# Kernel tuning notes

Measured on AMD Instinct MI355X. Metric: run time of the kernel, lower is better.

## Reference

```python
import jax, jax.numpy as jnp
import numpy as np

HIDDEN = 1024
HEADS = 16
HEAD_DIM = HIDDEN // HEADS  # 64
ROPE_DIM = 64
ROPE_BASE = 10000.0
B, T = 2, 2048


def setup_inputs() -> dict:
    key = jax.random.key(0)
    k1, k2, k3, k4, k5, k6 = jax.random.split(key, 6)
    x = jax.random.normal(k1, (B, T, HIDDEN), dtype=jnp.float32)
    input_ids = jax.random.randint(k2, (B, T), 0, 32000)
    # torch Linear weights: [out_features, in_features]
    qkv_w = jax.random.normal(k3, (3 * HIDDEN, HIDDEN), dtype=jnp.float32) * (1.0 / np.sqrt(HIDDEN))
    qkv_b = jnp.zeros((3 * HIDDEN,), dtype=jnp.float32)
    out_w = jax.random.normal(k4, (HIDDEN, HIDDEN), dtype=jnp.float32) * (1.0 / np.sqrt(HIDDEN))
    out_b = jnp.zeros((HIDDEN,), dtype=jnp.float32)
    global_idx = jnp.array([0, 1, 2], dtype=jnp.int64)  # special_tokens values
    return {"x": x, "input_ids": input_ids, "qkv_w": qkv_w, "qkv_b": qkv_b,
            "out_w": out_w, "out_b": out_b, "global_idx": global_idx}


def _rope_cos_sin(t, offset=0):
    inv_freq = 1.0 / (ROPE_BASE ** (jnp.arange(0, ROPE_DIM, 2, dtype=jnp.float32) / ROPE_DIM))  # [ROPE_DIM/2]
    pos = jnp.arange(offset, offset + t, dtype=jnp.float32)
    freqs = pos[:, None] * inv_freq[None, :]  # [T, ROPE_DIM/2]
    return jnp.cos(freqs)[None, None], jnp.sin(freqs)[None, None]  # [1,1,T,ROPE_DIM/2]


def _apply_rotary(x, cos, sin):
    x_rot, x_pass = x[..., :ROPE_DIM], x[..., ROPE_DIM:]
    half = ROPE_DIM // 2
    x1, x2 = x_rot[..., :half], x_rot[..., half:]
    return jnp.concatenate([x1 * cos - x2 * sin, x1 * sin + x2 * cos, x_pass], axis=-1)


def reference(x, input_ids, qkv_w, qkv_b, out_w, out_b, global_idx):
    b, t, _ = x.shape
    qkv = x @ qkv_w.T + qkv_b  # [B,T,3*HIDDEN]
    q, k, v = jnp.split(qkv, 3, axis=-1)
    # -> [B, H, T, Dh]
    reshape = lambda z: z.reshape(b, t, HEADS, HEAD_DIM).transpose(0, 2, 1, 3)
    q, k, v = reshape(q), reshape(k), reshape(v)
    cos, sin = _rope_cos_sin(t)
    q = _apply_rotary(q, cos, sin)
    k = _apply_rotary(k, cos, sin)
    # causal + global-query mask
    causal = jnp.tril(jnp.ones((t, t), dtype=bool))[None, None]  # [1,1,T,T]
    global_mask = jnp.isin(input_ids, global_idx)  # [B,T]
    allow = causal | global_mask[:, None, :, None]  # [B,1,T,T]
    scale = jnp.sqrt(jnp.float32(HEAD_DIM))
    logits = jnp.einsum('bhqd,bhkd->bhqk', q, k) / scale
    neg = -jnp.finfo(logits.dtype).max
    logits = jnp.where(allow, logits, neg)
    attn = jax.nn.softmax(logits, axis=-1)
    out = jnp.einsum('bhqk,bhkd->bhqd', attn, v)  # [B,H,T,Dh]
    out = out.transpose(0, 2, 1, 3).reshape(b, t, HEADS * HEAD_DIM)
    return out @ out_w.T + out_b
```

## Files before the change

kernel.cpp:

```cpp
#include <hip/hip_runtime.h>
#include <hip/hip_bf16.h>
#include <math.h>

typedef __bf16 bf16;
typedef __bf16 bf16x4 __attribute__((ext_vector_type(4)));
typedef __bf16 bf16x8 __attribute__((ext_vector_type(8)));
typedef float floatx4 __attribute__((ext_vector_type(4)));

#define HIDDEN 1024
#define NHEADS 16
#define HDIM 64
#define TSEQ 2048
#define NBATCH 2
#define MTOT (NBATCH * TSEQ)

__device__ inline void glds16(bf16* lds, const bf16* g)
{
  __builtin_amdgcn_global_load_lds(
      (const __attribute__((address_space(1))) unsigned int*)g,
      (__attribute__((address_space(3))) unsigned int*)lds, 16, 0, 0);
}

__global__ __launch_bounds__(256) void prep_kernel(
    const float* __restrict__ x, bf16* __restrict__ xb,
    const float* __restrict__ qkv_w, bf16* __restrict__ qkv_wb,
    float2* __restrict__ rope)
{
  const int bid = blockIdx.x;
  if (bid >= 3584) {
    const int e0 = ((bid - 3584) * 256 + threadIdx.x) * 4;
    const int t = e0 >> 5;
    const int d2 = e0 & 31;
#pragma unroll
    for (int j = 0; j < 4; j++) {
      const float inv = exp2f((float)(d2 + j) * -0.41524100f);
      float s, c;
      sincosf((float)t * inv, &s, &c);
      rope[e0 + j] = make_float2(c, s);
    }
    return;
  }
  const float* src = (bid < 2048) ? x : qkv_w;
  bf16* dst = (bid < 2048) ? xb : qkv_wb;
  const int i = (((bid < 2048) ? bid : bid - 2048) * 256 + threadIdx.x) * 8;
  const floatx4 u = *(const floatx4*)(src + i);
  const floatx4 v = *(const floatx4*)(src + i + 4);
  bf16x8 r;
#pragma unroll
  for (int j = 0; j < 4; j++) { r[j] = (bf16)u[j]; r[4 + j] = (bf16)v[j]; }
  *(bf16x8*)(dst + i) = r;
}

__global__ __launch_bounds__(256) void cvt_f32_bf16(
    const float* __restrict__ src, bf16* __restrict__ dst, int n)
{
  const int i = (blockIdx.x * 256 + threadIdx.x) * 8;
  if (i >= n) return;
  const floatx4 u = *(const floatx4*)(src + i);
  const floatx4 v = *(const floatx4*)(src + i + 4);
  bf16x8 r;
#pragma unroll
  for (int j = 0; j < 4; j++) { r[j] = (bf16)u[j]; r[4 + j] = (bf16)v[j]; }
  *(bf16x8*)(dst + i) = r;
}


#define GEMM_PROLOGUE()                                                     \
  const int tid  = threadIdx.x;                                             \
  const int lane = tid & 63;                                                \
  const int wv   = tid >> 6;                                                \
  const int quad = lane >> 4;                                               \
  const int l16  = lane & 15;                                               \
  const int m0 = blockIdx.y * 128;                                          \
  const int n0 = blockIdx.x * 128;                                          \
  const int wm = (wv >> 1) * 64;                                            \
  const int wn = (wv & 1) * 64;                                             \
  const int srow = lane >> 2;                                               \
  const int scol = ((lane & 3) ^ ((lane >> 3) & 3)) * 8;   \
  const int qsw  = (quad ^ ((l16 >> 1) & 3)) * 8;         \
  const bf16* ga0 = A + (size_t)(m0 + wv * 32 + srow) * K + scol;           \
  const bf16* gb0 = W + (size_t)(n0 + wv * 32 + srow) * K + scol;           \
  floatx4 acc[4][4];                                                        \
  _Pragma("unroll") for (int i = 0; i < 4; i++)                             \
      _Pragma("unroll") for (int j = 0; j < 4; j++)                         \
          acc[i][j] = (floatx4){0.f, 0.f, 0.f, 0.f};

#define STAGE(buf, kk)                                                      \
  glds16(&As[buf][(wv * 32) * 32], ga0 + (kk));                             \
  glds16(&As[buf][(wv * 32 + 16) * 32], ga0 + (size_t)16 * K + (kk));       \
  glds16(&Bs[buf][(wv * 32) * 32], gb0 + (kk));                             \
  glds16(&Bs[buf][(wv * 32 + 16) * 32], gb0 + (size_t)16 * K + (kk));

#define COMPUTE(buf)                                                        \
  {                                                                         \
    bf16x8 af[4], bfr[4];                                                   \
    _Pragma("unroll") for (int i = 0; i < 4; i++)                           \
        af[i] = *(const bf16x8*)(&As[buf][(wm + i * 16 + l16) * 32 + qsw]); \
    _Pragma("unroll") for (int j = 0; j < 4; j++)                           \
        bfr[j] = *(const bf16x8*)(&Bs[buf][(wn + j * 16 + l16) * 32 + qsw]);\
    _Pragma("unroll") for (int i = 0; i < 4; i++)                           \
        _Pragma("unroll") for (int j = 0; j < 4; j++)                       \
            acc[i][j] = __builtin_amdgcn_mfma_f32_16x16x32_bf16(            \
                af[i], bfr[j], acc[i][j], 0, 0, 0);                         \
  }

#define GEMM_MAIN_LOOP()                                                    \
  STAGE(0, 0);                                                              \
  STAGE(1, 32);                                                             \
  int cur = 0;                                                              \
  const int nsteps = K / 32;                                                \
  _Pragma("unroll 1") for (int t = 0; t < nsteps - 1; t++) {                \
    asm volatile("s_waitcnt vmcnt(4)" ::: "memory");                        \
    __builtin_amdgcn_s_barrier();                                           \
    if (t + 2 < nsteps) {                                                   \
      const int nb = (cur >= 1) ? cur - 1 : cur + 2;                        \
      STAGE(nb, (t + 2) * 32);                                              \
    }                                                                       \
    COMPUTE(cur);                                                           \
    cur = (cur == 2) ? 0 : cur + 1;                                         \
  }                                                                         \
  asm volatile("s_waitcnt vmcnt(0)" ::: "memory");                          \
  __builtin_amdgcn_s_barrier();                                             \
  COMPUTE(cur);

__global__ __launch_bounds__(256) void gemm_qkv(
    const bf16* __restrict__ A, const bf16* __restrict__ W,
    const float* __restrict__ bias, const float2* __restrict__ rope,
    bf16* __restrict__ Qb, bf16* __restrict__ Kb, bf16* __restrict__ Vt,
    int M, int N, int K)
{
  __shared__ bf16 As[3][128 * 32];
  __shared__ bf16 Bs[3][128 * 32];

  GEMM_PROLOGUE();
  GEMM_MAIN_LOOP();

  const int sect = n0 >> 10;
  const int hw   = ((n0 & 1023) + wn) >> 6;

  float bs[4];
#pragma unroll
  for (int j = 0; j < 4; j++) bs[j] = bias[n0 + wn + j * 16 + l16];

  if (sect < 2) {
    bf16* dst = sect ? Kb : Qb;
#pragma unroll
    for (int i = 0; i < 4; i++) {
      const int gmBase = m0 + wm + i * 16 + quad * 4;
#pragma unroll
      for (int r = 0; r < 4; r++) {
        const int gm = gmBase + r;
        const int b_ = gm >> 11, t = gm & 2047;
        const size_t rowbase = ((size_t)(b_ * NHEADS + hw) * TSEQ + t) * HDIM;
        const float2 cs0 = rope[t * 32 + l16];
        const float2 cs1 = rope[t * 32 + 16 + l16];
        const float x1a = acc[i][0][r] + bs[0];
        const float x2a = acc[i][2][r] + bs[2];
        const float x1b = acc[i][1][r] + bs[1];
        const float x2b = acc[i][3][r] + bs[3];
        dst[rowbase + l16]      = (bf16)(x1a * cs0.x - x2a * cs0.y);
        dst[rowbase + 32 + l16] = (bf16)(x1a * cs0.y + x2a * cs0.x);
        dst[rowbase + 16 + l16] = (bf16)(x1b * cs1.x - x2b * cs1.y);
        dst[rowbase + 48 + l16] = (bf16)(x1b * cs1.y + x2b * cs1.x);
      }
    }
  } else {
#pragma unroll
    for (int j = 0; j < 4; j++) {
      const int d = j * 16 + l16;
#pragma unroll
      for (int i = 0; i < 4; i++) {
        const int gmBase = m0 + wm + i * 16 + quad * 4;
        const int b_ = gmBase >> 11, t0 = gmBase & 2047;
        bf16x4 vv;
#pragma unroll
        for (int r = 0; r < 4; r++) vv[r] = (bf16)(acc[i][j][r] + bs[j]);
        *(bf16x4*)(Vt + ((size_t)((b_ * NHEADS + hw) * HDIM + d)) * TSEQ + t0) = vv;
      }
    }
  }
}

__global__ __launch_bounds__(256) void gemm_out(
    const bf16* __restrict__ A, const bf16* __restrict__ W,
    const float* __restrict__ bias, float* __restrict__ C,
    int M, int N, int K)
{
  __shared__ bf16 As[3][128 * 32];
  __shared__ bf16 Bs[3][128 * 32];

  GEMM_PROLOGUE();
  GEMM_MAIN_LOOP();

#pragma unroll
  for (int i = 0; i < 4; i++) {
    const int gmBase = m0 + wm + i * 16 + quad * 4;
#pragma unroll
    for (int j = 0; j < 4; j++) {
      const int gn = n0 + wn + j * 16 + l16;
      const float bsv = bias[gn];
#pragma unroll
      for (int r = 0; r < 4; r++)
        C[(size_t)(gmBase + r) * N + gn] = acc[i][j][r] + bsv;
    }
  }
}

__device__ inline int swz(int g) { return (g & ~7) | ((g ^ (g >> 3) ^ (g >> 6)) & 7); }

__global__ __launch_bounds__(256) void attn_kernel(
    const bf16* __restrict__ Q, const bf16* __restrict__ K,
    const bf16* __restrict__ Vt, bf16* __restrict__ O,
    const int* __restrict__ ids, const int* __restrict__ gidx)
{
  __shared__ bf16 Ks[4096];
  __shared__ bf16 Vs[4096];
  __shared__ int flags[4];

  const int tid  = threadIdx.x;
  const int lane = tid & 63;
  const int wv   = tid >> 6;
  const int quad = lane >> 4;
  const int l16  = lane & 15;

  const int xcd = blockIdx.x & 7;
  const int j   = blockIdx.x >> 3;
  const int bh  = xcd * 4 + (j >> 4);
  const int p   = j & 15;
  const int b  = bh >> 4;
  const int h  = bh & 15;

  const bf16* Qp = Q + (size_t)bh * TSEQ * HDIM;
  const bf16* Kp = K + (size_t)bh * TSEQ * HDIM;
  const bf16* Vp = Vt + (size_t)bh * HDIM * TSEQ;

  const int rK  = tid >> 3;
  const int dcK = tid & 7;
  const int gk = ((rK >> 2) & 1) * 128 + (dcK >> 2) * 64 +
                 ((dcK & 3) * 16 + (((rK >> 3) << 2) | (rK & 3)));
  const int kd0 = swz(gk) * 8, kd1 = swz(gk + 256) * 8;
  const int dV = tid >> 3;
  const int uV = tid & 7;
  const int gv = (uV >> 2) * 256 + (dV >> 4) * 64 + ((uV & 3) * 16 + (dV & 15));
  const int vd0 = swz(gv) * 8, vd1 = swz(gv + 128) * 8;

  const int g0v = gidx[0], g1v = gidx[1], g2v = gidx[2];

#pragma unroll
  for (int ph = 0; ph < 2; ph++) {
    const int qt = ph ? p : (31 - p);
    const int q0 = qt * 64 + wv * 16;

    const bf16x8 qf0 = *(const bf16x8*)(Qp + (size_t)(q0 + l16) * HDIM + quad * 8);
    const bf16x8 qf1 = *(const bf16x8*)(Qp + (size_t)(q0 + l16) * HDIM + 32 + quad * 8);

    const int myq = q0 + l16;
    const int myid = ids[b * TSEQ + myq];
    const int gl = (myid == g0v) | (myid == g1v) | (myid == g2v);
    flags[wv] = __any(gl);
    __syncthreads();
    const int anyg = flags[0] | flags[1] | flags[2] | flags[3];
    const int kmax = anyg ? TSEQ : (qt * 64 + 64);

    float lsum = 0.f;
    floatx4 o[4];
#pragma unroll
    for (int nt = 0; nt < 4; nt++) o[nt] = (floatx4){0.f, 0.f, 0.f, 0.f};

    bf16x8 kA = *(const bf16x8*)(Kp + tid * 8);
    bf16x8 kB = *(const bf16x8*)(Kp + 2048 + tid * 8);
    bf16x8 vA = *(const bf16x8*)(Vp + (size_t)dV * TSEQ + uV * 8);
    bf16x8 vB = *(const bf16x8*)(Vp + (size_t)(dV + 32) * TSEQ + uV * 8);

    for (int k0 = 0; k0 < kmax; k0 += 64) {
      __syncthreads();
      *(bf16x8*)(Ks + kd0) = kA;
      *(bf16x8*)(Ks + kd1) = kB;
      *(bf16x8*)(Vs + vd0) = vA;
      *(bf16x8*)(Vs + vd1) = vB;
      __syncthreads();

      if (k0 + 64 < kmax) {
        const bf16* kc = Kp + (size_t)(k0 + 64) * HDIM;
        kA = *(const bf16x8*)(kc + tid * 8);
        kB = *(const bf16x8*)(kc + 2048 + tid * 8);
        vA = *(const bf16x8*)(Vp + (size_t)dV * TSEQ + k0 + 64 + uV * 8);
        vB = *(const bf16x8*)(Vp + (size_t)(dV + 32) * TSEQ + k0 + 64 + uV * 8);
      }

#pragma unroll
      for (int g = 0; g < 2; g++) {
        const int kb = k0 + g * 32;
        const int rb = g * 256 + lane;
        const bf16x8 a00 = *(const bf16x8*)(Ks + swz(rb) * 8);
        const bf16x8 a01 = *(const bf16x8*)(Ks + swz(rb + 64) * 8);
        const bf16x8 a10 = *(const bf16x8*)(Ks + swz(rb + 128) * 8);
        const bf16x8 a11 = *(const bf16x8*)(Ks + swz(rb + 192) * 8);
        floatx4 s0 = (floatx4){0.f, 0.f, 0.f, 0.f};
        floatx4 s1 = (floatx4){0.f, 0.f, 0.f, 0.f};
        s0 = __builtin_amdgcn_mfma_f32_16x16x32_bf16(a00, qf0, s0, 0, 0, 0);
        s0 = __builtin_amdgcn_mfma_f32_16x16x32_bf16(a01, qf1, s0, 0, 0, 0);
        s1 = __builtin_amdgcn_mfma_f32_16x16x32_bf16(a10, qf0, s1, 0, 0, 0);
        s1 = __builtin_amdgcn_mfma_f32_16x16x32_bf16(a11, qf1, s1, 0, 0, 0);

        bf16x8 pf;
#pragma unroll
        for (int r = 0; r < 4; r++) {
          const int key0 = kb + quad * 8 + r;
          const int key1 = key0 + 4;
          const float p0 = (gl || key0 <= myq) ? __expf(s0[r] * 0.125f) : 0.f;
          const float p1 = (gl || key1 <= myq) ? __expf(s1[r] * 0.125f) : 0.f;
          lsum += p0 + p1;
          pf[r]     = (bf16)p0;
          pf[4 + r] = (bf16)p1;
        }

#pragma unroll
        for (int nt = 0; nt < 4; nt++) {
          const bf16x8 vf = *(const bf16x8*)(Vs + swz(g * 256 + nt * 64 + lane) * 8);
          o[nt] = __builtin_amdgcn_mfma_f32_16x16x32_bf16(pf, vf, o[nt], 0, 0, 0);
        }
      }
    }

    lsum += __shfl_xor(lsum, 16);
    lsum += __shfl_xor(lsum, 32);

#pragma unroll
    for (int r = 0; r < 4; r++) {
      const float inv = 1.0f / __shfl(lsum, quad * 4 + r);
      const int q = q0 + quad * 4 + r;
      const size_t rowoff = ((size_t)b * TSEQ + q) * HIDDEN + h * HDIM;
#pragma unroll
      for (int nt = 0; nt < 4; nt++)
        O[rowoff + nt * 16 + l16] = (bf16)(o[nt][r] * inv);
    }
  }
}

extern "C" void kernel_launch(void* const* d_in, const int* in_sizes, int n_in,
                              void* d_out, int out_size, void* d_ws, size_t ws_size,
                              hipStream_t stream)
{
  const float* x     = (const float*)d_in[0];
  const int*   ids   = (const int*)d_in[1];
  const float* qkv_w = (const float*)d_in[2];
  const float* qkv_b = (const float*)d_in[3];
  const float* out_w = (const float*)d_in[4];
  const float* out_b = (const float*)d_in[5];
  const int*   gidx  = (const int*)d_in[6];
  float* out = (float*)d_out;

  char* ws = (char*)d_ws;
  bf16* Q      = (bf16*)(ws);
  bf16* Kb     = (bf16*)(ws + (size_t)(8u << 20));
  bf16* Vt     = (bf16*)(ws + (size_t)(16u << 20));
  bf16* slot24 = (bf16*)(ws + (size_t)(24u << 20));
  bf16* xb     = slot24;
  bf16* O      = slot24;
  bf16* out_wb = (bf16*)(ws + (size_t)(16u << 20));
  bf16* qkv_wb = (bf16*)d_out;
  float2* rope = (float2*)((char*)d_out + (size_t)(6u << 20));

  prep_kernel<<<3648, 256, 0, stream>>>(x, xb, qkv_w, qkv_wb, rope);
  gemm_qkv<<<dim3(3072 / 128, MTOT / 128), 256, 0, stream>>>(
      xb, qkv_wb, qkv_b, rope, Q, Kb, Vt, MTOT, 3 * HIDDEN, HIDDEN);
  attn_kernel<<<512, 256, 0, stream>>>(Q, Kb, Vt, O, ids, gidx);
  cvt_f32_bf16<<<512, 256, 0, stream>>>(out_w, out_wb, HIDDEN * HIDDEN);
  gemm_out<<<dim3(HIDDEN / 128, MTOT / 128), 256, 0, stream>>>(
      O, out_wb, out_b, out, MTOT, HIDDEN, HIDDEN);
}
```

Baseline: 203.0 us.

## Remap GEMM blocks per XCD and halve out-projection N tile

Both GEMMs switch to a 1D grid whose block index is remapped so that blocks landing on the same XCD (assigned round-robin by blockIdx mod 8) cover a compact 2D region of the output. This is meant to improve L2 reuse of the A and W tiles within each XCD. The output-projection GEMM also moves from 128x128 to 128x64 tiles, doubling its grid to 512 blocks so the GPU's CUs are better occupied. The cost is more A-tile reloads and fewer MFMAs per LDS load in gemm_out, and the mapping is hardcoded to these exact grid shapes.

Result: faster. 198.7 us (-2.1%).

```diff
diff --git a/kernel.cpp b/kernel.cpp
--- a/kernel.cpp
+++ b/kernel.cpp
@@ -64,26 +64,6 @@
   *(bf16x8*)(dst + i) = r;
 }
 
-
-#define GEMM_PROLOGUE()                                                     \
-  const int tid  = threadIdx.x;                                             \
-  const int lane = tid & 63;                                                \
-  const int wv   = tid >> 6;                                                \
-  const int quad = lane >> 4;                                               \
-  const int l16  = lane & 15;                                               \
-  const int m0 = blockIdx.y * 128;                                          \
-  const int n0 = blockIdx.x * 128;                                          \
-  const int wm = (wv >> 1) * 64;                                            \
-  const int wn = (wv & 1) * 64;                                             \
-  const int srow = lane >> 2;                                               \
-  const int scol = ((lane & 3) ^ ((lane >> 3) & 3)) * 8;   \
-  const int qsw  = (quad ^ ((l16 >> 1) & 3)) * 8;         \
-  const bf16* ga0 = A + (size_t)(m0 + wv * 32 + srow) * K + scol;           \
-  const bf16* gb0 = W + (size_t)(n0 + wv * 32 + srow) * K + scol;           \
-  floatx4 acc[4][4];                                                        \
-  _Pragma("unroll") for (int i = 0; i < 4; i++)                             \
-      _Pragma("unroll") for (int j = 0; j < 4; j++)                         \
-          acc[i][j] = (floatx4){0.f, 0.f, 0.f, 0.f};
 
 #define STAGE(buf, kk)                                                      \
   glds16(&As[buf][(wv * 32) * 32], ga0 + (kk));                             \
@@ -104,25 +84,6 @@
                 af[i], bfr[j], acc[i][j], 0, 0, 0);                         \
   }
 
-#define GEMM_MAIN_LOOP()                                                    \
-  STAGE(0, 0);                                                              \
-  STAGE(1, 32);                                                             \
-  int cur = 0;                                                              \
-  const int nsteps = K / 32;                                                \
-  _Pragma("unroll 1") for (int t = 0; t < nsteps - 1; t++) {                \
-    asm volatile("s_waitcnt vmcnt(4)" ::: "memory");                        \
-    __builtin_amdgcn_s_barrier();                                           \
-    if (t + 2 < nsteps) {                                                   \
-      const int nb = (cur >= 1) ? cur - 1 : cur + 2;                        \
-      STAGE(nb, (t + 2) * 32);                                              \
-    }                                                                       \
-    COMPUTE(cur);                                                           \
-    cur = (cur == 2) ? 0 : cur + 1;                                         \
-  }                                                                         \
-  asm volatile("s_waitcnt vmcnt(0)" ::: "memory");                          \
-  __builtin_amdgcn_s_barrier();                                             \
-  COMPUTE(cur);
-
 __global__ __launch_bounds__(256) void gemm_qkv(
     const bf16* __restrict__ A, const bf16* __restrict__ W,
     const float* __restrict__ bias, const float2* __restrict__ rope,
@@ -132,8 +93,53 @@
   __shared__ bf16 As[3][128 * 32];
   __shared__ bf16 Bs[3][128 * 32];
 
-  GEMM_PROLOGUE();
-  GEMM_MAIN_LOOP();
+  const int tid  = threadIdx.x;
+  const int lane = tid & 63;
+  const int wv   = tid >> 6;
+  const int quad = lane >> 4;
+  const int l16  = lane & 15;
+
+  const int f   = blockIdx.x;
+  const int xcd = f & 7;
+  const int rr  = f >> 3;
+  const int bx  = (xcd & 1) * 12 + (rr % 12);
+  const int by  = (xcd >> 1) * 8 + (rr / 12);
+  const int m0 = by * 128;
+  const int n0 = bx * 128;
+
+  const int wm = (wv >> 1) * 64;
+  const int wn = (wv & 1) * 64;
+  const int srow = lane >> 2;
+  const int scol = ((lane & 3) ^ ((lane >> 3) & 3)) * 8;
+  const int qsw  = (quad ^ ((l16 >> 1) & 3)) * 8;
+
+  const bf16* ga0 = A + (size_t)(m0 + wv * 32 + srow) * K + scol;
+  const bf16* gb0 = W + (size_t)(n0 + wv * 32 + srow) * K + scol;
+
+  floatx4 acc[4][4];
+#pragma unroll
+  for (int i = 0; i < 4; i++)
+#pragma unroll
+    for (int j = 0; j < 4; j++) acc[i][j] = (floatx4){0.f, 0.f, 0.f, 0.f};
+
+  STAGE(0, 0);
+  STAGE(1, 32);
+  int cur = 0;
+  const int nsteps = K / 32;
+#pragma unroll 1
+  for (int t = 0; t < nsteps - 1; t++) {
+    asm volatile("s_waitcnt vmcnt(4)" ::: "memory");
+    __builtin_amdgcn_s_barrier();
+    if (t + 2 < nsteps) {
+      const int nb = (cur >= 1) ? cur - 1 : cur + 2;
+      STAGE(nb, (t + 2) * 32);
+    }
+    COMPUTE(cur);
+    cur = (cur == 2) ? 0 : cur + 1;
+  }
+  asm volatile("s_waitcnt vmcnt(0)" ::: "memory");
+  __builtin_amdgcn_s_barrier();
+  COMPUTE(cur);
 
   const int sect = n0 >> 10;
   const int hw   = ((n0 & 1023) + wn) >> 6;
@@ -187,17 +193,79 @@
     int M, int N, int K)
 {
   __shared__ bf16 As[3][128 * 32];
-  __shared__ bf16 Bs[3][128 * 32];
-
-  GEMM_PROLOGUE();
-  GEMM_MAIN_LOOP();
-
-#pragma unroll
-  for (int i = 0; i < 4; i++) {
+  __shared__ bf16 Bs[3][64 * 32];
+
+  const int tid  = threadIdx.x;
+  const int lane = tid & 63;
+  const int wv   = tid >> 6;
+  const int quad = lane >> 4;
+  const int l16  = lane & 15;
+
+  const int f   = blockIdx.x;
+  const int xcd = f & 7;
+  const int rr  = f >> 3;
+  const int bx  = (xcd & 1) * 8 + (rr & 7);
+  const int by  = (xcd >> 1) * 8 + (rr >> 3);
+  const int m0 = by * 128;
+  const int n0 = bx * 64;
+  const int wm = wv * 32;
+
+  const int srow = lane >> 2;
+  const int scol = ((lane & 3) ^ ((lane >> 3) & 3)) * 8;
+  const int qsw  = (quad ^ ((l16 >> 1) & 3)) * 8;
+
+  const bf16* ga0 = A + (size_t)(m0 + wv * 32 + srow) * K + scol;
+  const bf16* gb0 = W + (size_t)(n0 + wv * 16 + srow) * K + scol;
+
+  floatx4 acc[2][4];
+#pragma unroll
+  for (int i = 0; i < 2; i++)
+#pragma unroll
+    for (int j = 0; j < 4; j++) acc[i][j] = (floatx4){0.f, 0.f, 0.f, 0.f};
+
+#define STAGE_O(buf, kk)                                                    \
+  glds16(&As[buf][(wv * 32) * 32], ga0 + (kk));                             \
+  glds16(&As[buf][(wv * 32 + 16) * 32], ga0 + (size_t)16 * K + (kk));       \
+  glds16(&Bs[buf][(wv * 16) * 32], gb0 + (kk));
+
+#define COMPUTE_O(buf)                                                      \
+  {                                                                         \
+    bf16x8 af[2], bfr[4];                                                   \
+    _Pragma("unroll") for (int i = 0; i < 2; i++)                           \
+        af[i] = *(const bf16x8*)(&As[buf][(wm + i * 16 + l16) * 32 + qsw]); \
+    _Pragma("unroll") for (int j = 0; j < 4; j++)                           \
+        bfr[j] = *(const bf16x8*)(&Bs[buf][(j * 16 + l16) * 32 + qsw]);     \
+    _Pragma("unroll") for (int i = 0; i < 2; i++)                           \
+        _Pragma("unroll") for (int j = 0; j < 4; j++)                       \
+            acc[i][j] = __builtin_amdgcn_mfma_f32_16x16x32_bf16(            \
+                af[i], bfr[j], acc[i][j], 0, 0, 0);                         \
+  }
+
+  STAGE_O(0, 0);
+  STAGE_O(1, 32);
+  int cur = 0;
+  const int nsteps = K / 32;
+#pragma unroll 1
+  for (int t = 0; t < nsteps - 1; t++) {
+    asm volatile("s_waitcnt vmcnt(3)" ::: "memory");
+    __builtin_amdgcn_s_barrier();
+    if (t + 2 < nsteps) {
+      const int nb = (cur >= 1) ? cur - 1 : cur + 2;
+      STAGE_O(nb, (t + 2) * 32);
+    }
+    COMPUTE_O(cur);
+    cur = (cur == 2) ? 0 : cur + 1;
+  }
+  asm volatile("s_waitcnt vmcnt(0)" ::: "memory");
+  __builtin_amdgcn_s_barrier();
+  COMPUTE_O(cur);
+
+#pragma unroll
+  for (int i = 0; i < 2; i++) {
     const int gmBase = m0 + wm + i * 16 + quad * 4;
 #pragma unroll
     for (int j = 0; j < 4; j++) {
-      const int gn = n0 + wn + j * 16 + l16;
+      const int gn = n0 + j * 16 + l16;
       const float bsv = bias[gn];
 #pragma unroll
       for (int r = 0; r < 4; r++)
@@ -363,10 +431,10 @@
   float2* rope = (float2*)((char*)d_out + (size_t)(6u << 20));
 
   prep_kernel<<<3648, 256, 0, stream>>>(x, xb, qkv_w, qkv_wb, rope);
-  gemm_qkv<<<dim3(3072 / 128, MTOT / 128), 256, 0, stream>>>(
+  gemm_qkv<<<768, 256, 0, stream>>>(
       xb, qkv_wb, qkv_b, rope, Q, Kb, Vt, MTOT, 3 * HIDDEN, HIDDEN);
   attn_kernel<<<512, 256, 0, stream>>>(Q, Kb, Vt, O, ids, gidx);
   cvt_f32_bf16<<<512, 256, 0, stream>>>(out_w, out_wb, HIDDEN * HIDDEN);
-  gemm_out<<<dim3(HIDDEN / 128, MTOT / 128), 256, 0, stream>>>(
+  gemm_out<<<512, 256, 0, stream>>>(
       O, out_wb, out_b, out, MTOT, HIDDEN, HIDDEN);
 }
```
